# Kernel optimization log

Hardware: AMD Instinct MI355X
Metric: run time of the kernel (lower is better)

## Reference

```python
import jax, jax.numpy as jnp
import numpy as np

BETA = 0.9       # neuron_args['beta']
THRESH = 0.5     # neuron_args['threshold'] (mem_thresh)
ALPHA = 2.0      # surrogate.atan(alpha=2)
BIN = 50         # int(0.2 / 0.004)
NSTEPS = 7       # num_steps
STEP = BIN // NSTEPS  # 7 -> only buffer[:49] is used


@jax.custom_vjp
def atan_spike(x):
    return (x > 0).astype(x.dtype)

def _asp_fwd(x):
    return (x > 0).astype(x.dtype), x

def _asp_bwd(x, g):
    return (g * (ALPHA / 2.0) / (1.0 + (jnp.pi / 2.0 * ALPHA * x) ** 2),)

atan_spike.defvjp(_asp_fwd, _asp_bwd)


def _heaviside_detached(x):
    # snntorch mem_reset: reset = spike_grad(mem - thresh).detach()
    return jax.lax.stop_gradient((x > 0).astype(x.dtype))


def _forward(x, W_in, W_h0, W_out, v_x, v_y):
    T, B, D = x.shape
    H = W_in.shape[0]
    O = W_out.shape[0]
    vxy = jnp.concatenate([v_x, v_y])  # (2,)

    def single_forward(acc):  # acc: (NSTEPS, B, D)
        mem1 = jnp.zeros((B, H), x.dtype)
        mem2 = jnp.zeros((B, H), x.dtype)
        mem_out = jnp.zeros((B, O), x.dtype)
        for s in range(NSTEPS):
            cur = acc[s] @ W_in.T                      # (B, H); dropout in eval mode = identity
            reset = _heaviside_detached(mem1 - THRESH)
            mem1 = (BETA * mem1 + cur) * (1.0 - reset)  # reset_mechanism='zero'
            spk = atan_spike(mem1 - THRESH)
            cur = spk @ W_h0.T
            reset = _heaviside_detached(mem2 - THRESH)
            mem2 = (BETA * mem2 + cur) * (1.0 - reset)
            spk = atan_spike(mem2 - THRESH)
            cur = spk @ W_out.T                        # (B, O)
            mem_out = BETA * mem_out + cur             # reset_mechanism='none'
        return mem_out

    def step(carry, x_t):
        buf, L = carry  # buf: (BIN, B, D) zero-padded past L valid frames
        # torch: append then trim front when >BIN. While growing, frames keep
        # fixed positions with zeros at the end (NOT a sliding window yet).
        grow = jax.lax.dynamic_update_slice_in_dim(buf, x_t[None], L, 0)
        slide = jnp.concatenate([buf[1:], x_t[None]], axis=0)
        buf = jnp.where(L < BIN, grow, slide)
        L = jnp.minimum(L + 1, BIN)
        # acc_spikes[i] = sum(buf[7i : 7i+7]); frame 49 unused (49 = 7*7)
        acc = buf[: NSTEPS * STEP].reshape(NSTEPS, STEP, B, D).sum(axis=1)
        pred = single_forward(acc)                     # (B, 2)
        return (buf, L), pred * vxy

    init = (jnp.zeros((BIN, B, D), x.dtype), jnp.int32(1))  # one initial zero frame
    _, preds = jax.lax.scan(step, init, x)             # (T, B, 2)
    return preds


def setup_inputs() -> dict:
    key = jax.random.key(0)
    ks = jax.random.split(key, 6)
    T, B, D, H, O = 128, 1024, 96, 128, 2
    x = jax.random.uniform(ks[0], (T, B, D), dtype=jnp.float32)
    W_in = jax.random.normal(ks[1], (H, D), dtype=jnp.float32) / np.sqrt(D)
    W_h0 = jax.random.normal(ks[2], (H, H), dtype=jnp.float32) / np.sqrt(H)
    W_out = jax.random.normal(ks[3], (O, H), dtype=jnp.float32) / np.sqrt(H)
    v_x = jax.random.normal(ks[4], (1,), dtype=jnp.float32)
    v_y = jax.random.normal(ks[5], (1,), dtype=jnp.float32)
    return {"x": x, "W_in": W_in, "W_h0": W_h0, "W_out": W_out, "v_x": v_x, "v_y": v_y}


def reference(x, W_in, W_h0, W_out, v_x, v_y):
    return _forward(x, W_in, W_h0, W_out, v_x, v_y)
```

## Files before the change

kernel.cpp:

```cpp
#include <hip/hip_runtime.h>
#include <cstdint>

#define T_STEPS 128
#define BATCH   1024
#define D_INPUT 96
#define H_DIM   128
#define NWIN    163
#define BD      (BATCH * D_INPUT)

__device__ __forceinline__ int widx_for(int t, int s) {
    if (t >= 49) return t - 49 + 7 * s;
    if (s == 0)  return 121 + min(5, t);
    const int st = 7 * s - 1;
    if (t < st) return -1;
    const int len = min(7, t - st + 1);
    return (len == 7) ? st : (127 + (s - 1) * 6 + (len - 1));
}

__device__ __forceinline__ int swz_idx(int row, int col) {
    return (row << 7) | (col ^ ((row & 63) << 1));
}

__global__ __launch_bounds__(256) void kT_wint(const float* __restrict__ Win,
                                               const float* __restrict__ Wh0,
                                               float* __restrict__ WinT,
                                               float* __restrict__ Wh0T) {
    const int tid = threadIdx.x;
    if (blockIdx.x < 48) {
        const int e = blockIdx.x * 256 + tid;
        const int h = e / D_INPUT, d = e % D_INPUT;
        WinT[d * H_DIM + h] = Win[e];
    } else {
        const int e = (blockIdx.x - 48) * 256 + tid;
        const int i = e >> 7, h = e & 127;
        Wh0T[h * H_DIM + i] = Wh0[e];
    }
}

__global__ __launch_bounds__(256) void kA0_winsum(const float* __restrict__ x,
                                                  float* __restrict__ WS) {
    const int flat = blockIdx.x * 256 + threadIdx.x;
    float* wsp = WS + flat;
    float r[7];
#pragma unroll
    for (int t = 0; t < T_STEPS; ++t) {
        r[t % 7] = x[(size_t)t * BD + flat];
        if (t <= 5) {
            float s = r[0];
#pragma unroll
            for (int k = 1; k <= t; ++k) s = __fadd_rn(s, r[k % 7]);
            wsp[(size_t)(121 + t) * BD] = s;
        }
        if (t >= 6 && t <= 126) {
            const int w = t - 6;
            float s = r[w % 7];
#pragma unroll
            for (int k = 1; k < 7; ++k) s = __fadd_rn(s, r[(w + k) % 7]);
            wsp[(size_t)w * BD] = s;
        }
        if (t >= 6 && t <= 46) {
            const int sv = (t + 1) / 7;
            if (sv >= 1 && 7 * sv >= t - 4 && 7 * sv <= t + 1) {
                const int start = 7 * sv - 1;
                const int len = t - start + 1;
                float s = r[start % 7];
#pragma unroll
                for (int k = 1; k < len; ++k) s = __fadd_rn(s, r[(start + k) % 7]);
                wsp[(size_t)(127 + (sv - 1) * 6 + (len - 1)) * BD] = s;
            }
        }
    }
}

__global__ __launch_bounds__(256) void kA_wincur(const float* __restrict__ WS,
                                                 const float* __restrict__ WinT,
                                                 float* __restrict__ CUR1) {
    __shared__ float xs[D_INPUT * 32];
    __shared__ float wT[D_INPUT * H_DIM];
    const int widx = blockIdx.x;
    const int b0   = blockIdx.y * 32;
    const int tid  = threadIdx.x;

    {
        const float2* WinT2 = (const float2*)WinT;
        for (int e2 = tid; e2 < D_INPUT * (H_DIM / 2); e2 += 256) {
            const int d = e2 >> 6, h2 = e2 & 63;
            *(float2*)&wT[swz_idx(d, h2 << 1)] = WinT2[e2];
        }
    }
    for (int e = tid; e < D_INPUT * 32; e += 256) {
        const int d = e % D_INPUT, bq = e / D_INPUT;
        xs[d * 32 + bq] = WS[(size_t)widx * BD + (size_t)(b0 + bq) * D_INPUT + d];
    }
    __syncthreads();

    const int hp = tid & 63, g = tid >> 6;
    const int h0 = hp << 1;
    float acc[8][2];
#pragma unroll
    for (int r = 0; r < 8; ++r) { acc[r][0] = 0.f; acc[r][1] = 0.f; }

#pragma unroll 6
    for (int d = 0; d < D_INPUT; ++d) {
        const float2 wp  = *(const float2*)&wT[swz_idx(d, h0)];
        const float4 xv0 = *(const float4*)&xs[d * 32 + g * 8];
        const float4 xv1 = *(const float4*)&xs[d * 32 + g * 8 + 4];
        const float xv[8] = {xv0.x,xv0.y,xv0.z,xv0.w, xv1.x,xv1.y,xv1.z,xv1.w};
#pragma unroll
        for (int r = 0; r < 8; ++r) {
            acc[r][0] = __fmaf_rn(xv[r], wp.x, acc[r][0]);
            acc[r][1] = __fmaf_rn(xv[r], wp.y, acc[r][1]);
        }
    }
    float* op = CUR1 + ((size_t)widx * BATCH + b0 + g * 8) * H_DIM + h0;
#pragma unroll
    for (int r = 0; r < 8; ++r) {
        float2 o; o.x = acc[r][0]; o.y = acc[r][1];
        *(float2*)(op + (size_t)r * H_DIM) = o;
    }
}

__global__ __launch_bounds__(512, 2) void kB_snn(const float* __restrict__ CUR1,
                                                 const float* __restrict__ Wh0T,
                                                 const float* __restrict__ Wout,
                                                 const float* __restrict__ vxp,
                                                 const float* __restrict__ vyp,
                                                 float* __restrict__ out) {
    __shared__ float sf[8][64 * 32];
    const int tid = threadIdx.x;

    const int w = tid >> 6, lane = tid & 63;
    const int t  = blockIdx.y;
    const int i0 = lane << 1;
    float* sfw = sf[w];
    const int lbase = lane * 32;
    const float wex = Wout[i0],     wey = Wout[H_DIM + i0];
    const float wox = Wout[i0 + 1], woy = Wout[H_DIM + i0 + 1];
    const float vx = vxp[0], vy = vyp[0];
    const int b0 = (blockIdx.x << 7) + (w << 4);

    float m1a[16], m1b[16], m2a[16], m2b[16], poa[16], pob[16];
    float c1a[16], c1b[16];
    bool  s1a[16], s1b[16], s2a[16], s2b[16];
#pragma unroll
    for (int k = 0; k < 16; ++k) {
        m1a[k]=0.f; m1b[k]=0.f; m2a[k]=0.f; m2b[k]=0.f; poa[k]=0.f; pob[k]=0.f;
        s1a[k]=false; s1b[k]=false; s2a[k]=false; s2b[k]=false;
    }

    {
        const int wi = widx_for(t, 0);
#pragma unroll
        for (int k = 0; k < 16; ++k) {
            c1a[k] = 0.f; c1b[k] = 0.f;
            if (wi >= 0) {
                const float2 v = *(const float2*)
                    &CUR1[((size_t)wi * BATCH + b0 + k) * H_DIM + i0];
                c1a[k] = v.x; c1b[k] = v.y;
            }
        }
    }

#pragma unroll 1
    for (int s = 0; s < 7; ++s) {
        float sev[16], sov[16];
#pragma unroll
        for (int k = 0; k < 16; ++k) {
            m1a[k] = s1a[k] ? 0.f : __fadd_rn(__fmul_rn(0.9f, m1a[k]), c1a[k]);
            m1b[k] = s1b[k] ? 0.f : __fadd_rn(__fmul_rn(0.9f, m1b[k]), c1b[k]);
            s1a[k] = m1a[k] > 0.5f; s1b[k] = m1b[k] > 0.5f;
            sev[k] = s1a[k] ? 1.0f : 0.0f;
            sov[k] = s1b[k] ? 1.0f : 0.0f;
        }
#pragma unroll
        for (int c = 0; c < 4; ++c) {
            float4 v;
            v.x = sev[c*4]; v.y = sev[c*4+1]; v.z = sev[c*4+2]; v.w = sev[c*4+3];
            *(float4*)&sfw[lbase + ((c     ^ (lane & 7)) << 2)] = v;
            v.x = sov[c*4]; v.y = sov[c*4+1]; v.z = sov[c*4+2]; v.w = sov[c*4+3];
            *(float4*)&sfw[lbase + (((c+4) ^ (lane & 7)) << 2)] = v;
        }

        const int win = (s < 6) ? widx_for(t, s + 1) : -1;
#pragma unroll
        for (int k = 0; k < 16; ++k) {
            c1a[k] = 0.f; c1b[k] = 0.f;
            if (win >= 0) {
                const float2 v = *(const float2*)
                    &CUR1[((size_t)win * BATCH + b0 + k) * H_DIM + i0];
                c1a[k] = v.x; c1b[k] = v.y;
            }
        }

        float c2a[16], c2b[16];
#pragma unroll
        for (int k = 0; k < 16; ++k) { c2a[k] = 0.f; c2b[k] = 0.f; }
#pragma unroll 8
        for (int j = 0; j < 64; ++j) {
            const float2 we = *(const float2*)&Wh0T[(size_t)(2*j)     * H_DIM + i0];
            const float2 wo = *(const float2*)&Wh0T[(size_t)(2*j + 1) * H_DIM + i0];
            const int jb = j * 32, jx = (j & 7) << 2;
            const float4 e0 = *(const float4*)&sfw[jb + ((0  << 2) ^ jx)];
            const float4 e1 = *(const float4*)&sfw[jb + ((1  << 2) ^ jx)];
            const float4 e2 = *(const float4*)&sfw[jb + ((2  << 2) ^ jx)];
            const float4 e3 = *(const float4*)&sfw[jb + ((3  << 2) ^ jx)];
            const float4 o0 = *(const float4*)&sfw[jb + ((4  << 2) ^ jx)];
            const float4 o1 = *(const float4*)&sfw[jb + ((5  << 2) ^ jx)];
            const float4 o2 = *(const float4*)&sfw[jb + ((6  << 2) ^ jx)];
            const float4 o3 = *(const float4*)&sfw[jb + ((7  << 2) ^ jx)];
            const float se[16] = {e0.x,e0.y,e0.z,e0.w, e1.x,e1.y,e1.z,e1.w,
                                  e2.x,e2.y,e2.z,e2.w, e3.x,e3.y,e3.z,e3.w};
            const float so[16] = {o0.x,o0.y,o0.z,o0.w, o1.x,o1.y,o1.z,o1.w,
                                  o2.x,o2.y,o2.z,o2.w, o3.x,o3.y,o3.z,o3.w};
#pragma unroll
            for (int k = 0; k < 16; ++k) {
                c2a[k] = __fmaf_rn(se[k], we.x, c2a[k]);
                c2b[k] = __fmaf_rn(se[k], we.y, c2b[k]);
                c2a[k] = __fmaf_rn(so[k], wo.x, c2a[k]);
                c2b[k] = __fmaf_rn(so[k], wo.y, c2b[k]);
            }
        }

#pragma unroll
        for (int k = 0; k < 16; ++k) {
            m2a[k] = s2a[k] ? 0.f : __fadd_rn(__fmul_rn(0.9f, m2a[k]), c2a[k]);
            m2b[k] = s2b[k] ? 0.f : __fadd_rn(__fmul_rn(0.9f, m2b[k]), c2b[k]);
            s2a[k] = m2a[k] > 0.5f; s2b[k] = m2b[k] > 0.5f;
            const float p0 = (s2a[k] ? wex : 0.f) + (s2b[k] ? wox : 0.f);
            const float p1 = (s2a[k] ? wey : 0.f) + (s2b[k] ? woy : 0.f);
            poa[k] = __fmaf_rn(0.9f, poa[k], p0);
            pob[k] = __fmaf_rn(0.9f, pob[k], p1);
        }
    }

#pragma unroll
    for (int k = 0; k < 16; ++k) {
        float r0 = poa[k], r1 = pob[k];
#pragma unroll
        for (int off = 32; off > 0; off >>= 1) {
            r0 += __shfl_xor(r0, off);
            r1 += __shfl_xor(r1, off);
        }
        if (lane == 0) {
            float2 o;
            o.x = __fmul_rn(r0, vx);
            o.y = __fmul_rn(r1, vy);
            *(float2*)(out + ((size_t)t * BATCH + b0 + k) * 2) = o;
        }
    }
}

extern "C" void kernel_launch(void* const* d_in, const int* in_sizes, int n_in,
                              void* d_out, int out_size, void* d_ws, size_t ws_size,
                              hipStream_t stream) {
    const float* x    = (const float*)d_in[0];
    const float* Win  = (const float*)d_in[1];
    const float* Wh0  = (const float*)d_in[2];
    const float* Wout = (const float*)d_in[3];
    const float* vx   = (const float*)d_in[4];
    const float* vy   = (const float*)d_in[5];
    float* out  = (float*)d_out;

    float* CUR1 = (float*)d_ws;
    float* WS   = CUR1 + (size_t)NWIN * BATCH * H_DIM;
    float* WinT = WS   + (size_t)NWIN * BATCH * D_INPUT;
    float* Wh0T = WinT + (size_t)D_INPUT * H_DIM;

    kT_wint   <<<dim3(112),                 dim3(256), 0, stream>>>(Win, Wh0, WinT, Wh0T);
    kA0_winsum<<<dim3(BD / 256),            dim3(256), 0, stream>>>(x, WS);
    kA_wincur <<<dim3(NWIN, BATCH / 32),    dim3(256), 0, stream>>>(WS, WinT, CUR1);
    kB_snn    <<<dim3(BATCH / 128, T_STEPS), dim3(512), 0, stream>>>(CUR1, Wh0T, Wout, vx, vy, out);
}
```

Measured before the change: 932.0 us.

## Pack spikes as bf16 pairs in LDS and pre-pack Wh0 into float4 layout

Spike values (exactly 0 or 1) are now stored in shared memory as 16-bit bf16 halves packed two per 32-bit word. This halves the LDS footprint and the number of LDS reads in the layer-2 matmul inner loop. Wh0 is also pre-permuted so each lane fetches its even/odd weight pair with one float4 load instead of two float2 loads. The cost is extra shift/mask unpacking ALU work per inner iteration and a changed swizzle scheme.

New measurement: 1.007 ms. 8.0% more time.

```diff
diff --git a/kernel.cpp b/kernel.cpp
--- a/kernel.cpp
+++ b/kernel.cpp
@@ -24,7 +24,7 @@
 __global__ __launch_bounds__(256) void kT_wint(const float* __restrict__ Win,
                                                const float* __restrict__ Wh0,
                                                float* __restrict__ WinT,
-                                               float* __restrict__ Wh0T) {
+                                               float* __restrict__ Wh0P) {
     const int tid = threadIdx.x;
     if (blockIdx.x < 48) {
         const int e = blockIdx.x * 256 + tid;
@@ -32,8 +32,10 @@
         WinT[d * H_DIM + h] = Win[e];
     } else {
         const int e = (blockIdx.x - 48) * 256 + tid;
-        const int i = e >> 7, h = e & 127;
-        Wh0T[h * H_DIM + i] = Wh0[e];
+        const int f = e & 3, l = (e >> 2) & 63, j = e >> 8;
+        const int i = 2 * l + (f & 1);
+        const int h = 2 * j + (f >> 1);
+        Wh0P[e] = Wh0[i * H_DIM + h];
     }
 }
 
@@ -121,23 +123,24 @@
 }
 
 __global__ __launch_bounds__(512, 2) void kB_snn(const float* __restrict__ CUR1,
-                                                 const float* __restrict__ Wh0T,
+                                                 const float* __restrict__ Wh0P,
                                                  const float* __restrict__ Wout,
                                                  const float* __restrict__ vxp,
                                                  const float* __restrict__ vyp,
                                                  float* __restrict__ out) {
-    __shared__ float sf[8][64 * 32];
+    __shared__ uint32_t sf[8][1024];
     const int tid = threadIdx.x;
 
     const int w = tid >> 6, lane = tid & 63;
     const int t  = blockIdx.y;
     const int i0 = lane << 1;
-    float* sfw = sf[w];
-    const int lbase = lane * 32;
+    uint32_t* sfu = sf[w];
     const float wex = Wout[i0],     wey = Wout[H_DIM + i0];
     const float wox = Wout[i0 + 1], woy = Wout[H_DIM + i0 + 1];
     const float vx = vxp[0], vy = vyp[0];
     const int b0 = (blockIdx.x << 7) + (w << 4);
+    const int swl = (lane >> 1) & 3;
+    uint32_t* pub = sfu + lane * 16;
 
     float m1a[16], m1b[16], m2a[16], m2b[16], poa[16], pob[16];
     float c1a[16], c1b[16];
@@ -163,22 +166,31 @@
 
 #pragma unroll 1
     for (int s = 0; s < 7; ++s) {
-        float sev[16], sov[16];
-#pragma unroll
-        for (int k = 0; k < 16; ++k) {
-            m1a[k] = s1a[k] ? 0.f : __fadd_rn(__fmul_rn(0.9f, m1a[k]), c1a[k]);
-            m1b[k] = s1b[k] ? 0.f : __fadd_rn(__fmul_rn(0.9f, m1b[k]), c1b[k]);
-            s1a[k] = m1a[k] > 0.5f; s1b[k] = m1b[k] > 0.5f;
-            sev[k] = s1a[k] ? 1.0f : 0.0f;
-            sov[k] = s1b[k] ? 1.0f : 0.0f;
+        uint32_t tok[16];
+#pragma unroll
+        for (int m = 0; m < 8; ++m) {
+            float na0 = __fadd_rn(__fmul_rn(0.9f, m1a[2*m  ]), c1a[2*m  ]);
+            float nb0 = __fadd_rn(__fmul_rn(0.9f, m1b[2*m  ]), c1b[2*m  ]);
+            float na1 = __fadd_rn(__fmul_rn(0.9f, m1a[2*m+1]), c1a[2*m+1]);
+            float nb1 = __fadd_rn(__fmul_rn(0.9f, m1b[2*m+1]), c1b[2*m+1]);
+            m1a[2*m  ] = s1a[2*m  ] ? 0.f : na0;
+            m1b[2*m  ] = s1b[2*m  ] ? 0.f : nb0;
+            m1a[2*m+1] = s1a[2*m+1] ? 0.f : na1;
+            m1b[2*m+1] = s1b[2*m+1] ? 0.f : nb1;
+            s1a[2*m  ] = m1a[2*m  ] > 0.5f;  s1b[2*m  ] = m1b[2*m  ] > 0.5f;
+            s1a[2*m+1] = m1a[2*m+1] > 0.5f;  s1b[2*m+1] = m1b[2*m+1] > 0.5f;
+            const uint32_t t0 = s1a[2*m  ] ? 0x3F80u : 0u;
+            const uint32_t t1 = s1a[2*m+1] ? 0x3F80u : 0u;
+            const uint32_t u0 = s1b[2*m  ] ? 0x3F80u : 0u;
+            const uint32_t u1 = s1b[2*m+1] ? 0x3F80u : 0u;
+            tok[m]     = t0 | (t1 << 16);
+            tok[8 + m] = u0 | (u1 << 16);
         }
 #pragma unroll
         for (int c = 0; c < 4; ++c) {
-            float4 v;
-            v.x = sev[c*4]; v.y = sev[c*4+1]; v.z = sev[c*4+2]; v.w = sev[c*4+3];
-            *(float4*)&sfw[lbase + ((c     ^ (lane & 7)) << 2)] = v;
-            v.x = sov[c*4]; v.y = sov[c*4+1]; v.z = sov[c*4+2]; v.w = sov[c*4+3];
-            *(float4*)&sfw[lbase + (((c+4) ^ (lane & 7)) << 2)] = v;
+            uint4 v;
+            v.x = tok[c*4]; v.y = tok[c*4+1]; v.z = tok[c*4+2]; v.w = tok[c*4+3];
+            *(uint4*)&pub[((c ^ swl) << 2)] = v;
         }
 
         const int win = (s < 6) ? widx_for(t, s + 1) : -1;
@@ -197,27 +209,29 @@
         for (int k = 0; k < 16; ++k) { c2a[k] = 0.f; c2b[k] = 0.f; }
 #pragma unroll 8
         for (int j = 0; j < 64; ++j) {
-            const float2 we = *(const float2*)&Wh0T[(size_t)(2*j)     * H_DIM + i0];
-            const float2 wo = *(const float2*)&Wh0T[(size_t)(2*j + 1) * H_DIM + i0];
-            const int jb = j * 32, jx = (j & 7) << 2;
-            const float4 e0 = *(const float4*)&sfw[jb + ((0  << 2) ^ jx)];
-            const float4 e1 = *(const float4*)&sfw[jb + ((1  << 2) ^ jx)];
-            const float4 e2 = *(const float4*)&sfw[jb + ((2  << 2) ^ jx)];
-            const float4 e3 = *(const float4*)&sfw[jb + ((3  << 2) ^ jx)];
-            const float4 o0 = *(const float4*)&sfw[jb + ((4  << 2) ^ jx)];
-            const float4 o1 = *(const float4*)&sfw[jb + ((5  << 2) ^ jx)];
-            const float4 o2 = *(const float4*)&sfw[jb + ((6  << 2) ^ jx)];
-            const float4 o3 = *(const float4*)&sfw[jb + ((7  << 2) ^ jx)];
-            const float se[16] = {e0.x,e0.y,e0.z,e0.w, e1.x,e1.y,e1.z,e1.w,
-                                  e2.x,e2.y,e2.z,e2.w, e3.x,e3.y,e3.z,e3.w};
-            const float so[16] = {o0.x,o0.y,o0.z,o0.w, o1.x,o1.y,o1.z,o1.w,
-                                  o2.x,o2.y,o2.z,o2.w, o3.x,o3.y,o3.z,o3.w};
+            const float4 wv = *(const float4*)&Wh0P[((size_t)j * 64 + lane) * 4];
+            const int swj = (j >> 1) & 3;
+            const uint32_t* pj = sfu + j * 16;
+            const uint4 q0 = *(const uint4*)&pj[((0 ^ swj) << 2)];
+            const uint4 q1 = *(const uint4*)&pj[((1 ^ swj) << 2)];
+            const uint4 q2 = *(const uint4*)&pj[((2 ^ swj) << 2)];
+            const uint4 q3 = *(const uint4*)&pj[((3 ^ swj) << 2)];
+            const uint32_t wd[16] = {q0.x,q0.y,q0.z,q0.w, q1.x,q1.y,q1.z,q1.w,
+                                     q2.x,q2.y,q2.z,q2.w, q3.x,q3.y,q3.z,q3.w};
+            float se[16], so[16];
+#pragma unroll
+            for (int m = 0; m < 8; ++m) {
+                se[2*m  ] = __uint_as_float(wd[m]     << 16);
+                se[2*m+1] = __uint_as_float(wd[m]     & 0xFFFF0000u);
+                so[2*m  ] = __uint_as_float(wd[8 + m] << 16);
+                so[2*m+1] = __uint_as_float(wd[8 + m] & 0xFFFF0000u);
+            }
 #pragma unroll
             for (int k = 0; k < 16; ++k) {
-                c2a[k] = __fmaf_rn(se[k], we.x, c2a[k]);
-                c2b[k] = __fmaf_rn(se[k], we.y, c2b[k]);
-                c2a[k] = __fmaf_rn(so[k], wo.x, c2a[k]);
-                c2b[k] = __fmaf_rn(so[k], wo.y, c2b[k]);
+                c2a[k] = __fmaf_rn(se[k], wv.x, c2a[k]);
+                c2b[k] = __fmaf_rn(se[k], wv.y, c2b[k]);
+                c2a[k] = __fmaf_rn(so[k], wv.z, c2a[k]);
+                c2b[k] = __fmaf_rn(so[k], wv.w, c2b[k]);
             }
         }
 
@@ -264,10 +278,10 @@
     float* CUR1 = (float*)d_ws;
     float* WS   = CUR1 + (size_t)NWIN * BATCH * H_DIM;
     float* WinT = WS   + (size_t)NWIN * BATCH * D_INPUT;
-    float* Wh0T = WinT + (size_t)D_INPUT * H_DIM;
-
-    kT_wint   <<<dim3(112),                 dim3(256), 0, stream>>>(Win, Wh0, WinT, Wh0T);
+    float* Wh0P = WinT + (size_t)D_INPUT * H_DIM;
+
+    kT_wint   <<<dim3(112),                 dim3(256), 0, stream>>>(Win, Wh0, WinT, Wh0P);
     kA0_winsum<<<dim3(BD / 256),            dim3(256), 0, stream>>>(x, WS);
     kA_wincur <<<dim3(NWIN, BATCH / 32),    dim3(256), 0, stream>>>(WS, WinT, CUR1);
-    kB_snn    <<<dim3(BATCH / 128, T_STEPS), dim3(512), 0, stream>>>(CUR1, Wh0T, Wout, vx, vy, out);
-}
+    kB_snn    <<<dim3(BATCH / 128, T_STEPS), dim3(512), 0, stream>>>(CUR1, Wh0P, Wout, vx, vy, out);
+}
```

## Retile second-layer matmul to 8 batch x 4 hidden register tile per lane

Applied to the files above, without the earlier changes.

Changes the per-lane register tile of the spike @ Wh0 product in the SNN kernel from 16 batch rows x 2 hidden units to 8 batch rows x 4 hidden units. Wh0 is pre-permuted into a packed layout so each lane loads two float4 weights per j, and only 4 float4 LDS spike reads are needed per j instead of 8. This lowers shared-memory traffic per FMA and shrinks the membrane-2 state arrays. The output reduction now uses 32-lane shuffles per half-wave, and the spike-tile swizzle reads may now hit more LDS bank conflicts.

New measurement: 828.9 us. 11.1% less time.

```diff
diff --git a/kernel.cpp b/kernel.cpp
--- a/kernel.cpp
+++ b/kernel.cpp
@@ -24,7 +24,7 @@
 __global__ __launch_bounds__(256) void kT_wint(const float* __restrict__ Win,
                                                const float* __restrict__ Wh0,
                                                float* __restrict__ WinT,
-                                               float* __restrict__ Wh0T) {
+                                               float* __restrict__ Wh0Q) {
     const int tid = threadIdx.x;
     if (blockIdx.x < 48) {
         const int e = blockIdx.x * 256 + tid;
@@ -32,8 +32,8 @@
         WinT[d * H_DIM + h] = Win[e];
     } else {
         const int e = (blockIdx.x - 48) * 256 + tid;
-        const int i = e >> 7, h = e & 127;
-        Wh0T[h * H_DIM + i] = Wh0[e];
+        const int r = e & 3, p = (e >> 2) & 1, q = (e >> 3) & 31, j = e >> 8;
+        Wh0Q[e] = Wh0[(4 * q + r) * H_DIM + (2 * j + p)];
     }
 }
 
@@ -121,7 +121,7 @@
 }
 
 __global__ __launch_bounds__(512, 2) void kB_snn(const float* __restrict__ CUR1,
-                                                 const float* __restrict__ Wh0T,
+                                                 const float* __restrict__ Wh0Q,
                                                  const float* __restrict__ Wout,
                                                  const float* __restrict__ vxp,
                                                  const float* __restrict__ vyp,
@@ -132,20 +132,29 @@
     const int w = tid >> 6, lane = tid & 63;
     const int t  = blockIdx.y;
     const int i0 = lane << 1;
+    const int g  = lane >> 5;
+    const int q  = lane & 31;
+    const int iq = q << 2;
     float* sfw = sf[w];
     const int lbase = lane * 32;
-    const float wex = Wout[i0],     wey = Wout[H_DIM + i0];
-    const float wox = Wout[i0 + 1], woy = Wout[H_DIM + i0 + 1];
+    const float4 wex4 = *(const float4*)&Wout[iq];
+    const float4 wey4 = *(const float4*)&Wout[H_DIM + iq];
     const float vx = vxp[0], vy = vyp[0];
     const int b0 = (blockIdx.x << 7) + (w << 4);
 
-    float m1a[16], m1b[16], m2a[16], m2b[16], poa[16], pob[16];
-    float c1a[16], c1b[16];
-    bool  s1a[16], s1b[16], s2a[16], s2b[16];
+    float m1a[16], m1b[16], c1a[16], c1b[16];
+    bool  s1a[16], s1b[16];
+    float m2[8][4], po0[8], po1[8];
+    bool  s2[8][4];
 #pragma unroll
     for (int k = 0; k < 16; ++k) {
-        m1a[k]=0.f; m1b[k]=0.f; m2a[k]=0.f; m2b[k]=0.f; poa[k]=0.f; pob[k]=0.f;
-        s1a[k]=false; s1b[k]=false; s2a[k]=false; s2b[k]=false;
+        m1a[k]=0.f; m1b[k]=0.f; s1a[k]=false; s1b[k]=false;
+    }
+#pragma unroll
+    for (int b = 0; b < 8; ++b) {
+        po0[b]=0.f; po1[b]=0.f;
+#pragma unroll
+        for (int r = 0; r < 4; ++r) { m2[b][r]=0.f; s2[b][r]=false; }
     }
 
     {
@@ -192,60 +201,64 @@
             }
         }
 
-        float c2a[16], c2b[16];
-#pragma unroll
-        for (int k = 0; k < 16; ++k) { c2a[k] = 0.f; c2b[k] = 0.f; }
+        float c2[8][4];
+#pragma unroll
+        for (int b = 0; b < 8; ++b)
+#pragma unroll
+            for (int r = 0; r < 4; ++r) c2[b][r] = 0.f;
+
 #pragma unroll 8
         for (int j = 0; j < 64; ++j) {
-            const float2 we = *(const float2*)&Wh0T[(size_t)(2*j)     * H_DIM + i0];
-            const float2 wo = *(const float2*)&Wh0T[(size_t)(2*j + 1) * H_DIM + i0];
+            const float4 we4 = *(const float4*)&Wh0Q[((size_t)(j * 32 + q)) * 8];
+            const float4 wo4 = *(const float4*)&Wh0Q[((size_t)(j * 32 + q)) * 8 + 4];
             const int jb = j * 32, jx = (j & 7) << 2;
-            const float4 e0 = *(const float4*)&sfw[jb + ((0  << 2) ^ jx)];
-            const float4 e1 = *(const float4*)&sfw[jb + ((1  << 2) ^ jx)];
-            const float4 e2 = *(const float4*)&sfw[jb + ((2  << 2) ^ jx)];
-            const float4 e3 = *(const float4*)&sfw[jb + ((3  << 2) ^ jx)];
-            const float4 o0 = *(const float4*)&sfw[jb + ((4  << 2) ^ jx)];
-            const float4 o1 = *(const float4*)&sfw[jb + ((5  << 2) ^ jx)];
-            const float4 o2 = *(const float4*)&sfw[jb + ((6  << 2) ^ jx)];
-            const float4 o3 = *(const float4*)&sfw[jb + ((7  << 2) ^ jx)];
-            const float se[16] = {e0.x,e0.y,e0.z,e0.w, e1.x,e1.y,e1.z,e1.w,
-                                  e2.x,e2.y,e2.z,e2.w, e3.x,e3.y,e3.z,e3.w};
-            const float so[16] = {o0.x,o0.y,o0.z,o0.w, o1.x,o1.y,o1.z,o1.w,
-                                  o2.x,o2.y,o2.z,o2.w, o3.x,o3.y,o3.z,o3.w};
-#pragma unroll
-            for (int k = 0; k < 16; ++k) {
-                c2a[k] = __fmaf_rn(se[k], we.x, c2a[k]);
-                c2b[k] = __fmaf_rn(se[k], we.y, c2b[k]);
-                c2a[k] = __fmaf_rn(so[k], wo.x, c2a[k]);
-                c2b[k] = __fmaf_rn(so[k], wo.y, c2b[k]);
-            }
-        }
-
-#pragma unroll
-        for (int k = 0; k < 16; ++k) {
-            m2a[k] = s2a[k] ? 0.f : __fadd_rn(__fmul_rn(0.9f, m2a[k]), c2a[k]);
-            m2b[k] = s2b[k] ? 0.f : __fadd_rn(__fmul_rn(0.9f, m2b[k]), c2b[k]);
-            s2a[k] = m2a[k] > 0.5f; s2b[k] = m2b[k] > 0.5f;
-            const float p0 = (s2a[k] ? wex : 0.f) + (s2b[k] ? wox : 0.f);
-            const float p1 = (s2a[k] ? wey : 0.f) + (s2b[k] ? woy : 0.f);
-            poa[k] = __fmaf_rn(0.9f, poa[k], p0);
-            pob[k] = __fmaf_rn(0.9f, pob[k], p1);
-        }
-    }
-
-#pragma unroll
-    for (int k = 0; k < 16; ++k) {
-        float r0 = poa[k], r1 = pob[k];
-#pragma unroll
-        for (int off = 32; off > 0; off >>= 1) {
+            const float4 E0 = *(const float4*)&sfw[jb + (((2*g    ) << 2) ^ jx)];
+            const float4 E1 = *(const float4*)&sfw[jb + (((2*g + 1) << 2) ^ jx)];
+            const float4 O0 = *(const float4*)&sfw[jb + (((2*g + 4) << 2) ^ jx)];
+            const float4 O1 = *(const float4*)&sfw[jb + (((2*g + 5) << 2) ^ jx)];
+            const float sevj[8] = {E0.x,E0.y,E0.z,E0.w, E1.x,E1.y,E1.z,E1.w};
+            const float sovj[8] = {O0.x,O0.y,O0.z,O0.w, O1.x,O1.y,O1.z,O1.w};
+            const float wev[4] = {we4.x, we4.y, we4.z, we4.w};
+            const float wov[4] = {wo4.x, wo4.y, wo4.z, wo4.w};
+#pragma unroll
+            for (int b = 0; b < 8; ++b) {
+#pragma unroll
+                for (int r = 0; r < 4; ++r) {
+                    c2[b][r] = __fmaf_rn(sevj[b], wev[r], c2[b][r]);
+                    c2[b][r] = __fmaf_rn(sovj[b], wov[r], c2[b][r]);
+                }
+            }
+        }
+
+#pragma unroll
+        for (int b = 0; b < 8; ++b) {
+            float p0 = 0.f, p1 = 0.f;
+#pragma unroll
+            for (int r = 0; r < 4; ++r) {
+                m2[b][r] = s2[b][r] ? 0.f
+                         : __fadd_rn(__fmul_rn(0.9f, m2[b][r]), c2[b][r]);
+                s2[b][r] = m2[b][r] > 0.5f;
+                p0 += s2[b][r] ? ((const float*)&wex4)[r] : 0.f;
+                p1 += s2[b][r] ? ((const float*)&wey4)[r] : 0.f;
+            }
+            po0[b] = __fmaf_rn(0.9f, po0[b], p0);
+            po1[b] = __fmaf_rn(0.9f, po1[b], p1);
+        }
+    }
+
+#pragma unroll
+    for (int b = 0; b < 8; ++b) {
+        float r0 = po0[b], r1 = po1[b];
+#pragma unroll
+        for (int off = 16; off > 0; off >>= 1) {
             r0 += __shfl_xor(r0, off);
             r1 += __shfl_xor(r1, off);
         }
-        if (lane == 0) {
+        if (q == 0) {
             float2 o;
             o.x = __fmul_rn(r0, vx);
             o.y = __fmul_rn(r1, vy);
-            *(float2*)(out + ((size_t)t * BATCH + b0 + k) * 2) = o;
+            *(float2*)(out + ((size_t)t * BATCH + b0 + g * 8 + b) * 2) = o;
         }
     }
 }
@@ -264,10 +277,10 @@
     float* CUR1 = (float*)d_ws;
     float* WS   = CUR1 + (size_t)NWIN * BATCH * H_DIM;
     float* WinT = WS   + (size_t)NWIN * BATCH * D_INPUT;
-    float* Wh0T = WinT + (size_t)D_INPUT * H_DIM;
-
-    kT_wint   <<<dim3(112),                 dim3(256), 0, stream>>>(Win, Wh0, WinT, Wh0T);
+    float* Wh0Q = WinT + (size_t)D_INPUT * H_DIM;
+
+    kT_wint   <<<dim3(112),                 dim3(256), 0, stream>>>(Win, Wh0, WinT, Wh0Q);
     kA0_winsum<<<dim3(BD / 256),            dim3(256), 0, stream>>>(x, WS);
     kA_wincur <<<dim3(NWIN, BATCH / 32),    dim3(256), 0, stream>>>(WS, WinT, CUR1);
-    kB_snn    <<<dim3(BATCH / 128, T_STEPS), dim3(512), 0, stream>>>(CUR1, Wh0T, Wout, vx, vy, out);
-}
+    kB_snn    <<<dim3(BATCH / 128, T_STEPS), dim3(512), 0, stream>>>(CUR1, Wh0Q, Wout, vx, vy, out);
+}
```
